# Kernel optimization log

Hardware: AMD Instinct MI355X
Metric: run time of the kernel (lower is better)

The kernel has to match this reference:

```python
import jax, jax.numpy as jnp
import numpy as np

D_MODEL = 768
N_HEADS = 12
D_FF = 3072
EPS = 1e-5


def _layernorm(x, g, b):
    mu = jnp.mean(x, axis=-1, keepdims=True)
    var = jnp.mean(jnp.square(x - mu), axis=-1, keepdims=True)
    return (x - mu) * jax.lax.rsqrt(var + EPS) * g + b


def setup_inputs() -> dict:
    key = jax.random.key(0)
    ks = jax.random.split(key, 16)
    d, f = D_MODEL, D_FF
    s = 1.0 / np.sqrt(d)
    inp = {
        "x": jax.random.normal(ks[0], (1, 4096, d), dtype=jnp.float32),
        "Wq": jax.random.normal(ks[1], (d, d), dtype=jnp.float32) * s,
        "bq": jnp.zeros((d,), jnp.float32),
        "Wk": jax.random.normal(ks[2], (d, d), dtype=jnp.float32) * s,
        "bk": jnp.zeros((d,), jnp.float32),
        "Wv": jax.random.normal(ks[3], (d, d), dtype=jnp.float32) * s,
        "bv": jnp.zeros((d,), jnp.float32),
        "Wo": jax.random.normal(ks[4], (d, d), dtype=jnp.float32) * s,
        "bo": jnp.zeros((d,), jnp.float32),
        "ln1_g": jnp.ones((d,), jnp.float32),
        "ln1_b": jnp.zeros((d,), jnp.float32),
        "ln2_g": jnp.ones((d,), jnp.float32),
        "ln2_b": jnp.zeros((d,), jnp.float32),
        "W1": jax.random.normal(ks[5], (d, f), dtype=jnp.float32) * s,
        "b1": jnp.zeros((f,), jnp.float32),
        "W2": jax.random.normal(ks[6], (f, d), dtype=jnp.float32) * (1.0 / np.sqrt(f)),
        "b2": jnp.zeros((d,), jnp.float32),
    }
    return inp


def reference(x, Wq, bq, Wk, bk, Wv, bv, Wo, bo, ln1_g, ln1_b, ln2_g, ln2_b, W1, b1, W2, b2):
    b, s, d = x.shape
    h = N_HEADS
    dk = d // h

    # --- attention sublayer (pre-norm residual) ---
    xn = _layernorm(x, ln1_g, ln1_b)

    def proj(W, bias):
        y = xn @ W + bias                      # [b, s, d]
        return y.reshape(b, s, h, dk).transpose(0, 2, 1, 3)  # [b, h, s, dk]

    q, k, v = proj(Wq, bq), proj(Wk, bk), proj(Wv, bv)
    scores = jnp.einsum("bhqd,bhkd->bhqk", q, k) / np.sqrt(dk)
    attn = jax.nn.softmax(scores, axis=-1)
    ctx = jnp.einsum("bhqk,bhkd->bhqd", attn, v)
    ctx = ctx.transpose(0, 2, 1, 3).reshape(b, s, d)
    x = x + (ctx @ Wo + bo)

    # --- FFN sublayer (pre-norm residual) ---
    xn2 = _layernorm(x, ln2_g, ln2_b)
    ff = jax.nn.gelu(xn2 @ W1 + b1, approximate=False) @ W2 + b2
    return x + ff
```

## Files before the change

### kernel.cpp

```cpp
#include <hip/hip_runtime.h>
#include <hip/hip_bf16.h>

typedef __attribute__((ext_vector_type(8))) __bf16 bf16x8;
typedef __attribute__((ext_vector_type(4))) __bf16 bf16x4;
typedef __attribute__((ext_vector_type(4))) float f32x4;
typedef __attribute__((ext_vector_type(4))) unsigned short u16x4;
typedef __attribute__((ext_vector_type(8))) unsigned short u16x8;
typedef unsigned short ushort_t;

__device__ __forceinline__ ushort_t f2bf(float f) {
    union { float f; unsigned u; } v; v.f = f;
    unsigned r = v.u + 0x7fffu + ((v.u >> 16) & 1u);
    return (ushort_t)(r >> 16);
}

__device__ __forceinline__ void gload16(const ushort_t* g, ushort_t* l) {
    __builtin_amdgcn_global_load_lds(
        (const __attribute__((address_space(1))) unsigned int*)g,
        (__attribute__((address_space(3))) unsigned int*)l,
        16, 0, 0);
}

__device__ __forceinline__ void ln_row(const float* __restrict__ xr,
                                       const float* __restrict__ g,
                                       const float* __restrict__ b,
                                       ushort_t* __restrict__ orow, int t) {
    float v0 = xr[t], v1 = xr[t + 256], v2 = xr[t + 512];
    float s  = v0 + v1 + v2;
    float s2 = v0 * v0 + v1 * v1 + v2 * v2;
#pragma unroll
    for (int off = 32; off; off >>= 1) {
        s  += __shfl_down(s, off);
        s2 += __shfl_down(s2, off);
    }
    __shared__ float red[8];
    const int wid = t >> 6, lane = t & 63;
    if (lane == 0) { red[wid] = s; red[4 + wid] = s2; }
    __syncthreads();
    __shared__ float stats[2];
    if (t == 0) {
        float S = red[0] + red[1] + red[2] + red[3];
        float S2 = red[4] + red[5] + red[6] + red[7];
        float mu = S * (1.0f / 768.0f);
        float var = S2 * (1.0f / 768.0f) - mu * mu;
        stats[0] = mu;
        stats[1] = rsqrtf(var + 1e-5f);
    }
    __syncthreads();
    const float mu = stats[0], rs = stats[1];
    orow[t]       = f2bf((v0 - mu) * rs * g[t]       + b[t]);
    orow[t + 256] = f2bf((v1 - mu) * rs * g[t + 256] + b[t + 256]);
    orow[t + 512] = f2bf((v2 - mu) * rs * g[t + 512] + b[t + 512]);
}

__global__ __launch_bounds__(256) void ln_kernel(const float* __restrict__ x,
                                                 const float* __restrict__ g,
                                                 const float* __restrict__ b,
                                                 ushort_t* __restrict__ out) {
    const int row = blockIdx.x;
    ln_row(x + (size_t)row * 768, g, b, out + (size_t)row * 768, threadIdx.x);
}

__global__ __launch_bounds__(256) void prep_ln(
    const float* __restrict__ Wq, const float* __restrict__ Wk,
    const float* __restrict__ Wv, const float* __restrict__ Wo,
    const float* __restrict__ W1, const float* __restrict__ W2,
    const float* __restrict__ bq, const float* __restrict__ bk,
    const float* __restrict__ bv,
    const float* __restrict__ x, const float* __restrict__ ln1_g,
    const float* __restrict__ ln1_b,
    ushort_t* __restrict__ WqkvT, ushort_t* __restrict__ WoT,
    ushort_t* __restrict__ W1T, ushort_t* __restrict__ W2T,
    float* __restrict__ bqkv, ushort_t* __restrict__ xn) {
    const int bid = blockIdx.x;
    const int t = threadIdx.x;
    if (bid >= 6915) {
        const int row = bid - 6915;
        ln_row(x + (size_t)row * 768, ln1_g, ln1_b, xn + (size_t)row * 768, t);
        return;
    }
    if (bid >= 6912) {
        const int i = bid - 6912;
        const float* s = (i == 0) ? bq : (i == 1) ? bk : bv;
#pragma unroll
        for (int j = t; j < 768; j += 256) bqkv[i * 768 + j] = s[j];
        return;
    }
    const float* src; ushort_t* dst; int R, C, ti;
    if (bid < 576)       { src = Wq; dst = WqkvT;               R = 768;  C = 768;  ti = bid; }
    else if (bid < 1152) { src = Wk; dst = WqkvT + 768 * 768;   R = 768;  C = 768;  ti = bid - 576; }
    else if (bid < 1728) { src = Wv; dst = WqkvT + 2 * 768 * 768; R = 768; C = 768; ti = bid - 1152; }
    else if (bid < 2304) { src = Wo; dst = WoT;                 R = 768;  C = 768;  ti = bid - 1728; }
    else if (bid < 4608) { src = W1; dst = W1T;                 R = 768;  C = 3072; ti = bid - 2304; }
    else                 { src = W2; dst = W2T;                 R = 3072; C = 768;  ti = bid - 4608; }
    const int tpr = C >> 5;
    const int c0 = (ti % tpr) * 32, r0 = (ti / tpr) * 32;
    __shared__ float tile[32][33];
    {
        const int c = t & 31, r = t >> 5;
#pragma unroll
        for (int i = 0; i < 4; i++)
            tile[r + i * 8][c] = src[(size_t)(r0 + r + i * 8) * C + c0 + c];
    }
    __syncthreads();
    {
        const int oc = t >> 3, q = t & 7;
        u16x4 o;
#pragma unroll
        for (int k = 0; k < 4; k++) o[k] = f2bf(tile[q * 4 + k][oc]);
        *(u16x4*)&dst[(size_t)(c0 + oc) * R + r0 + q * 4] = o;
    }
}

template <int GELU, int RES, int OUTF, int OUTB, int OUTV>
__global__ __launch_bounds__(256, 3)
void gemm64(const ushort_t* __restrict__ A, const ushort_t* __restrict__ Bt,
            const float* __restrict__ bias, const float* __restrict__ res,
            float* __restrict__ outF, ushort_t* __restrict__ outB, int ldo,
            ushort_t* __restrict__ outV,
            int M, int N, int K) {
    constexpr int TR = 192, BK = 64, LL = 6;
    __shared__ __align__(16) ushort_t Ls[2][TR * BK];

    const int nbx = gridDim.x;
    const int nwg = nbx * gridDim.y;
    int fb = blockIdx.y * nbx + blockIdx.x;
    fb = (fb & 7) * (nwg >> 3) + (fb >> 3);
    const int m0 = (fb / nbx) * 128, n0 = (fb % nbx) * 64;

    const int t = threadIdx.x;
    const int wid = t >> 6, lane = t & 63;
    const int wr = wid >> 1, wc = wid & 1;
    const int row16 = lane & 15, kg = lane >> 4;
    const int rsw = row16 & 7;

    const int srow = lane >> 3;
    const int sslot = (lane & 7) ^ srow;
    const ushort_t* gsrc[LL];
    int lofs[LL];
#pragma unroll
    for (int i = 0; i < LL; i++) {
        const int r0 = wid * 48 + 8 * i;
        gsrc[i] = (r0 < 128 ? A + (size_t)(m0 + r0 + srow) * K
                            : Bt + (size_t)(n0 + r0 - 128 + srow) * K) + sslot * 8;
        lofs[i] = r0 * BK;
    }

#define STAGEP(buf, kofs) do {                                       \
        _Pragma("unroll")                                            \
        for (int i = 0; i < LL; i++)                                 \
            gload16(gsrc[i] + (kofs), &Ls[buf][lofs[i]]);            \
    } while (0)

    f32x4 acc[4][2] = {};
    const int NS = K >> 6;
    STAGEP(0, 0);
    STAGEP(1, BK);
    int cur = 0;

    for (int s = 0; s < NS; ++s) {
        if (s + 1 == NS) asm volatile("s_waitcnt vmcnt(0)" ::: "memory");
        else             asm volatile("s_waitcnt vmcnt(%0)" :: "i"(LL) : "memory");
        __builtin_amdgcn_s_barrier();

        bf16x8 a[2][4], b[2][2];
#pragma unroll
        for (int kk = 0; kk < 2; kk++) {
            const int sA = ((kk * 4 + kg) ^ rsw) * 8;
#pragma unroll
            for (int i = 0; i < 4; i++)
                a[kk][i] = *(const bf16x8*)&Ls[cur][(wr * 64 + i * 16 + row16) * BK + sA];
#pragma unroll
            for (int j = 0; j < 2; j++)
                b[kk][j] = *(const bf16x8*)&Ls[cur][(128 + wc * 32 + j * 16 + row16) * BK + sA];
        }
        asm volatile("s_waitcnt lgkmcnt(0)" ::: "memory");
        __builtin_amdgcn_s_barrier();
        if (s + 2 < NS) STAGEP(cur, (s + 2) * BK);

        __builtin_amdgcn_s_setprio(1);
#pragma unroll
        for (int kk = 0; kk < 2; kk++)
#pragma unroll
            for (int i = 0; i < 4; i++)
#pragma unroll
                for (int j = 0; j < 2; j++)
                    acc[i][j] = __builtin_amdgcn_mfma_f32_16x16x32_bf16(a[kk][i], b[kk][j], acc[i][j], 0, 0, 0);
        __builtin_amdgcn_s_setprio(0);
        cur ^= 1;
    }
#undef STAGEP

#pragma unroll
    for (int i = 0; i < 4; i++)
#pragma unroll
        for (int j = 0; j < 2; j++) {
            const int col = n0 + wc * 32 + j * 16 + row16;
            const float bv = bias[col];
            const int rb = m0 + wr * 64 + i * 16 + kg * 4;
            if (OUTV && col >= 1536) {
                bf16x4 pk;
#pragma unroll
                for (int r = 0; r < 4; r++) pk[r] = (__bf16)(acc[i][j][r] + bv);
                *(bf16x4*)&outV[(size_t)(col - 1536) * 4096 + rb] = pk;
            } else {
#pragma unroll
                for (int r = 0; r < 4; r++) {
                    const int row = rb + r;
                    float v = acc[i][j][r] + bv;
                    if (GELU) {
                        float u = v + 0.044715f * v * v * v;
                        float e = __builtin_amdgcn_exp2f(2.30220779f * u);
                        v = v * e * __builtin_amdgcn_rcpf(e + 1.0f);
                    }
                    if (OUTV && col < 768) v *= 0.18033688011112042f;
                    if (RES) v += res[(size_t)row * N + col];
                    if (OUTF) outF[(size_t)row * N + col] = v;
                    if (OUTB) outB[(size_t)row * ldo + col] = f2bf(v);
                }
            }
        }
}

__device__ __forceinline__ int swz(int row, int col) {
    return row * 64 + (col ^ ((row & 7) << 3));
}

__global__ __launch_bounds__(256, 3)
void attn_kernel(const ushort_t* __restrict__ qk,
                 const ushort_t* __restrict__ Vt,
                 ushort_t* __restrict__ num0, ushort_t* __restrict__ num1,
                 float* __restrict__ den) {
    int fb = blockIdx.y * 32 + blockIdx.x;
    fb = (fb & 7) * 96 + (fb >> 3);
    const int q0 = (fb & 31) * 128;
    const int hs = fb >> 5;
    const int h = hs >> 1, sp = hs & 1;
    const int kt0 = sp * 32;

    const int t  = threadIdx.x;
    const int w = t >> 6, lane = t & 63;
    const int row16 = lane & 15, kg = lane >> 4;
    const int kb = kg * 8;

    __shared__ __align__(16) ushort_t Ps[128 * 64];
    __shared__ __align__(16) ushort_t Ks[2][64 * 64];
    __shared__ __align__(16) ushort_t Vs[2][64 * 64];

    {
        const int qr = t >> 1, cb = (t & 1) * 32;
        const size_t qbase = (size_t)(q0 + qr) * 1536 + h * 64 + cb;
#pragma unroll
        for (int j = 0; j < 4; j++)
            *(uint4*)&Ps[swz(qr, cb + j * 8)] = *(const uint4*)&qk[qbase + j * 8];
    }
    {
        const int sr = t >> 2, sc = (t & 3) * 8;
        const size_t kbase = (size_t)(kt0 * 64 + sr) * 1536 + 768 + h * 64 + sc;
        *(uint4*)&Ks[0][swz(sr, sc)]      = *(const uint4*)&qk[kbase];
        *(uint4*)&Ks[0][swz(sr, sc + 32)] = *(const uint4*)&qk[kbase + 32];
        const size_t vbase = (size_t)(h * 64 + sr) * 4096 + kt0 * 64 + sc;
        *(uint4*)&Vs[0][swz(sr, sc)]      = *(const uint4*)&Vt[vbase];
        *(uint4*)&Vs[0][swz(sr, sc + 32)] = *(const uint4*)&Vt[vbase + 32];
    }
    bf16x8 qa0[2], qa1[2];
#pragma unroll
    for (int qb = 0; qb < 2; qb++) {
        qa0[qb] = *(const bf16x8*)&Ps[swz(w * 32 + qb * 16 + row16, kb)];
        qa1[qb] = *(const bf16x8*)&Ps[swz(w * 32 + qb * 16 + row16, 32 + kb)];
    }
    __syncthreads();

    const int rr = lane >> 3;
    const int gcol = ((lane & 7) ^ rr) * 8;
    const ushort_t* gK = qk + 768 + h * 64 + gcol + (size_t)(w * 16 + rr) * 1536;
    const ushort_t* gV = Vt + (size_t)(h * 64 + w * 16 + rr) * 4096 + gcol;

    bf16x8 vones;
#pragma unroll
    for (int i = 0; i < 8; i++) vones[i] = (__bf16)1.0f;

    f32x4 o_acc[2][4] = {};
    f32x4 o_l[2] = {};
    int cur = 0;

    for (int it = 0; it < 32; ++it) {
        if (it != 31) {
            const int kv1 = (kt0 + it + 1) * 64;
            ushort_t* kd = &Ks[cur ^ 1][w * 1024];
            ushort_t* vd = &Vs[cur ^ 1][w * 1024];
            gload16(gK + (size_t)kv1 * 1536,       kd);
            gload16(gK + (size_t)(kv1 + 8) * 1536, kd + 512);
            gload16(gV + kv1,                      vd);
            gload16(gV + kv1 + 8 * 4096,           vd + 512);
        }

        const ushort_t* Kc = Ks[cur];
        const ushort_t* Vc = Vs[cur];

        bf16x8 ka0[4], ka1[4];
#pragma unroll
        for (int f = 0; f < 4; f++) {
            ka0[f] = *(const bf16x8*)&Kc[swz(f * 16 + row16, kb)];
            ka1[f] = *(const bf16x8*)&Kc[swz(f * 16 + row16, 32 + kb)];
        }

        f32x4 s_acc[2][4];
        __builtin_amdgcn_s_setprio(1);
#pragma unroll
        for (int qb = 0; qb < 2; qb++)
#pragma unroll
            for (int f = 0; f < 4; f++) {
                f32x4 z = {};
                z = __builtin_amdgcn_mfma_f32_16x16x32_bf16(ka0[f], qa0[qb], z, 0, 0, 0);
                s_acc[qb][f] = __builtin_amdgcn_mfma_f32_16x16x32_bf16(ka1[f], qa1[qb], z, 0, 0, 0);
            }
        __builtin_amdgcn_s_setprio(0);

#pragma unroll
        for (int qb = 0; qb < 2; qb++)
#pragma unroll
            for (int f = 0; f < 4; f++) {
                bf16x4 pk;
#pragma unroll
                for (int r = 0; r < 4; r++)
                    pk[r] = (__bf16)__builtin_amdgcn_exp2f(fminf(s_acc[qb][f][r], 30.0f));
                *(bf16x4*)&Ps[swz(w * 32 + qb * 16 + row16, f * 16 + kg * 4)] = pk;
            }

        bf16x8 pa0[2], pa1[2];
#pragma unroll
        for (int qb = 0; qb < 2; qb++) {
            pa0[qb] = *(const bf16x8*)&Ps[swz(w * 32 + qb * 16 + row16, kb)];
            pa1[qb] = *(const bf16x8*)&Ps[swz(w * 32 + qb * 16 + row16, 32 + kb)];
        }
        __builtin_amdgcn_s_setprio(1);
#pragma unroll
        for (int f = 0; f < 4; f++) {
            bf16x8 vb0 = *(const bf16x8*)&Vc[swz(f * 16 + row16, kb)];
            bf16x8 vb1 = *(const bf16x8*)&Vc[swz(f * 16 + row16, 32 + kb)];
#pragma unroll
            for (int qb = 0; qb < 2; qb++) {
                o_acc[qb][f] = __builtin_amdgcn_mfma_f32_16x16x32_bf16(pa0[qb], vb0, o_acc[qb][f], 0, 0, 0);
                o_acc[qb][f] = __builtin_amdgcn_mfma_f32_16x16x32_bf16(pa1[qb], vb1, o_acc[qb][f], 0, 0, 0);
            }
        }
#pragma unroll
        for (int qb = 0; qb < 2; qb++) {
            o_l[qb] = __builtin_amdgcn_mfma_f32_16x16x32_bf16(pa0[qb], vones, o_l[qb], 0, 0, 0);
            o_l[qb] = __builtin_amdgcn_mfma_f32_16x16x32_bf16(pa1[qb], vones, o_l[qb], 0, 0, 0);
        }
        __builtin_amdgcn_s_setprio(0);

        __syncthreads();
        cur ^= 1;
    }

    ushort_t* np = sp ? num1 : num0;
#pragma unroll
    for (int qb = 0; qb < 2; qb++)
#pragma unroll
        for (int f = 0; f < 4; f++)
#pragma unroll
            for (int r = 0; r < 4; r++) {
                const int qrow = q0 + w * 32 + qb * 16 + kg * 4 + r;
                np[(size_t)qrow * 768 + h * 64 + f * 16 + row16] = f2bf(o_acc[qb][f][r]);
            }
    if (row16 == 0) {
#pragma unroll
        for (int qb = 0; qb < 2; qb++)
#pragma unroll
            for (int r = 0; r < 4; r++) {
                const int qrow = q0 + w * 32 + qb * 16 + kg * 4 + r;
                den[((size_t)sp * 12 + h) * 4096 + qrow] = o_l[qb][r];
            }
    }
}

__global__ __launch_bounds__(256) void attn_combine(
    const ushort_t* __restrict__ num0, const ushort_t* __restrict__ num1,
    const float* __restrict__ den, ushort_t* __restrict__ ctx) {
    const int idx = blockIdx.x * 256 + threadIdx.x;
    const int q = idx / 96;
    const int g = idx % 96;
    const int h = g >> 3;
    const float rd = __builtin_amdgcn_rcpf(den[(size_t)h * 4096 + q] +
                                           den[((size_t)12 + h) * 4096 + q]);
    const size_t o = (size_t)q * 768 + g * 8;
    u16x8 a = *(const u16x8*)&num0[o];
    u16x8 b = *(const u16x8*)&num1[o];
    u16x8 pk;
#pragma unroll
    for (int i = 0; i < 8; i++) {
        const float av = __uint_as_float((unsigned)a[i] << 16);
        const float bv = __uint_as_float((unsigned)b[i] << 16);
        pk[i] = f2bf((av + bv) * rd);
    }
    *(u16x8*)&ctx[o] = pk;
}

extern "C" void kernel_launch(void* const* d_in, const int* in_sizes, int n_in,
                              void* d_out, int out_size, void* d_ws, size_t ws_size,
                              hipStream_t stream) {
    const float* x     = (const float*)d_in[0];
    const float* Wq    = (const float*)d_in[1];
    const float* bq    = (const float*)d_in[2];
    const float* Wk    = (const float*)d_in[3];
    const float* bk    = (const float*)d_in[4];
    const float* Wv    = (const float*)d_in[5];
    const float* bv    = (const float*)d_in[6];
    const float* Wo    = (const float*)d_in[7];
    const float* bo    = (const float*)d_in[8];
    const float* ln1_g = (const float*)d_in[9];
    const float* ln1_b = (const float*)d_in[10];
    const float* ln2_g = (const float*)d_in[11];
    const float* ln2_b = (const float*)d_in[12];
    const float* W1    = (const float*)d_in[13];
    const float* b1    = (const float*)d_in[14];
    const float* W2    = (const float*)d_in[15];
    const float* b2    = (const float*)d_in[16];

    char* ws = (char*)d_ws;
    ushort_t* WqkvT = (ushort_t*)ws; ws += (size_t)2304 * 768 * 2;
    ushort_t* WoT   = (ushort_t*)ws; ws += (size_t)768 * 768 * 2;
    ushort_t* W1T   = (ushort_t*)ws; ws += (size_t)3072 * 768 * 2;
    ushort_t* W2T   = (ushort_t*)ws; ws += (size_t)768 * 3072 * 2;
    float*    bqkv  = (float*)ws;    ws += (size_t)2304 * 4;
    ushort_t* xn    = (ushort_t*)ws; ws += (size_t)4096 * 768 * 2;
    ushort_t* qk    = (ushort_t*)ws; ws += (size_t)4096 * 1536 * 2;
    ushort_t* Vtb   = (ushort_t*)ws; ws += (size_t)768 * 4096 * 2;
    ushort_t* ctxb  = (ushort_t*)ws; ws += (size_t)4096 * 768 * 2;
    float*    x1    = (float*)ws;    ws += (size_t)4096 * 768 * 4;
    ushort_t* num0b = (ushort_t*)ws; ws += (size_t)4096 * 768 * 2;
    ushort_t* num1b = (ushort_t*)ws; ws += (size_t)4096 * 768 * 2;
    float*    den   = (float*)ws;    ws += (size_t)2 * 12 * 4096 * 4;
    ushort_t* H     = qk;

    prep_ln<<<6915 + 4096, 256, 0, stream>>>(Wq, Wk, Wv, Wo, W1, W2, bq, bk, bv,
                                             x, ln1_g, ln1_b,
                                             WqkvT, WoT, W1T, W2T, bqkv, xn);

    gemm64<0, 0, 0, 1, 1><<<dim3(36, 32), 256, 0, stream>>>(
        xn, WqkvT, bqkv, nullptr, nullptr, qk, 1536, Vtb, 4096, 2304, 768);

    attn_kernel<<<dim3(32, 24), 256, 0, stream>>>(qk, Vtb, num0b, num1b, den);
    attn_combine<<<1536, 256, 0, stream>>>(num0b, num1b, den, ctxb);

    gemm64<0, 1, 1, 0, 0><<<dim3(12, 32), 256, 0, stream>>>(
        ctxb, WoT, bo, x, x1, nullptr, 0, nullptr, 4096, 768, 768);

    ln_kernel<<<4096, 256, 0, stream>>>(x1, ln2_g, ln2_b, xn);
    gemm64<1, 0, 0, 1, 0><<<dim3(48, 32), 256, 0, stream>>>(
        xn, W1T, b1, nullptr, nullptr, H, 3072, nullptr, 4096, 3072, 768);
    gemm64<0, 1, 1, 0, 0><<<dim3(12, 32), 256, 0, stream>>>(
        H, W2T, b2, x1, (float*)d_out, nullptr, 0, nullptr, 4096, 768, 3072);

    (void)in_sizes; (void)n_in; (void)out_size; (void)ws_size;
}
```

Baseline: 190.1 us.

## Split attention KV range four ways and drop double-buffered K/V staging

The attention kernel now splits each head's key range into four chunks instead of two, doubling the grid to 1536 blocks. K/V shared memory drops from double-buffered to single-buffered, with the next tile's async load issued between two barriers after compute, and launch bounds rise to 4 blocks per CU. The combine kernel sums four partial numerators and denominators. This is meant to raise occupancy and parallelism, but it loses the overlap of loads with compute, adds a barrier per iteration, and doubles the partial-result traffic through the combine step.

```diff
diff --git a/kernel.cpp b/kernel.cpp
--- a/kernel.cpp
+++ b/kernel.cpp
@@ -226,17 +226,17 @@
     return row * 64 + (col ^ ((row & 7) << 3));
 }
 
-__global__ __launch_bounds__(256, 3)
+__global__ __launch_bounds__(256, 4)
 void attn_kernel(const ushort_t* __restrict__ qk,
                  const ushort_t* __restrict__ Vt,
-                 ushort_t* __restrict__ num0, ushort_t* __restrict__ num1,
+                 ushort_t* __restrict__ num,
                  float* __restrict__ den) {
     int fb = blockIdx.y * 32 + blockIdx.x;
-    fb = (fb & 7) * 96 + (fb >> 3);
+    fb = (fb & 7) * 192 + (fb >> 3);
     const int q0 = (fb & 31) * 128;
     const int hs = fb >> 5;
-    const int h = hs >> 1, sp = hs & 1;
-    const int kt0 = sp * 32;
+    const int h = hs >> 2, sp = hs & 3;
+    const int kt0 = sp * 16;
 
     const int t  = threadIdx.x;
     const int w = t >> 6, lane = t & 63;
@@ -244,8 +244,8 @@
     const int kb = kg * 8;
 
     __shared__ __align__(16) ushort_t Ps[128 * 64];
-    __shared__ __align__(16) ushort_t Ks[2][64 * 64];
-    __shared__ __align__(16) ushort_t Vs[2][64 * 64];
+    __shared__ __align__(16) ushort_t Ks[64 * 64];
+    __shared__ __align__(16) ushort_t Vs[64 * 64];
 
     {
         const int qr = t >> 1, cb = (t & 1) * 32;
@@ -257,11 +257,11 @@
     {
         const int sr = t >> 2, sc = (t & 3) * 8;
         const size_t kbase = (size_t)(kt0 * 64 + sr) * 1536 + 768 + h * 64 + sc;
-        *(uint4*)&Ks[0][swz(sr, sc)]      = *(const uint4*)&qk[kbase];
-        *(uint4*)&Ks[0][swz(sr, sc + 32)] = *(const uint4*)&qk[kbase + 32];
+        *(uint4*)&Ks[swz(sr, sc)]      = *(const uint4*)&qk[kbase];
+        *(uint4*)&Ks[swz(sr, sc + 32)] = *(const uint4*)&qk[kbase + 32];
         const size_t vbase = (size_t)(h * 64 + sr) * 4096 + kt0 * 64 + sc;
-        *(uint4*)&Vs[0][swz(sr, sc)]      = *(const uint4*)&Vt[vbase];
-        *(uint4*)&Vs[0][swz(sr, sc + 32)] = *(const uint4*)&Vt[vbase + 32];
+        *(uint4*)&Vs[swz(sr, sc)]      = *(const uint4*)&Vt[vbase];
+        *(uint4*)&Vs[swz(sr, sc + 32)] = *(const uint4*)&Vt[vbase + 32];
     }
     bf16x8 qa0[2], qa1[2];
 #pragma unroll
@@ -282,27 +282,13 @@
 
     f32x4 o_acc[2][4] = {};
     f32x4 o_l[2] = {};
-    int cur = 0;
-
-    for (int it = 0; it < 32; ++it) {
-        if (it != 31) {
-            const int kv1 = (kt0 + it + 1) * 64;
-            ushort_t* kd = &Ks[cur ^ 1][w * 1024];
-            ushort_t* vd = &Vs[cur ^ 1][w * 1024];
-            gload16(gK + (size_t)kv1 * 1536,       kd);
-            gload16(gK + (size_t)(kv1 + 8) * 1536, kd + 512);
-            gload16(gV + kv1,                      vd);
-            gload16(gV + kv1 + 8 * 4096,           vd + 512);
-        }
-
-        const ushort_t* Kc = Ks[cur];
-        const ushort_t* Vc = Vs[cur];
-
+
+    for (int it = 0; it < 16; ++it) {
         bf16x8 ka0[4], ka1[4];
 #pragma unroll
         for (int f = 0; f < 4; f++) {
-            ka0[f] = *(const bf16x8*)&Kc[swz(f * 16 + row16, kb)];
-            ka1[f] = *(const bf16x8*)&Kc[swz(f * 16 + row16, 32 + kb)];
+            ka0[f] = *(const bf16x8*)&Ks[swz(f * 16 + row16, kb)];
+            ka1[f] = *(const bf16x8*)&Ks[swz(f * 16 + row16, 32 + kb)];
         }
 
         f32x4 s_acc[2][4];
@@ -337,8 +323,8 @@
         __builtin_amdgcn_s_setprio(1);
 #pragma unroll
         for (int f = 0; f < 4; f++) {
-            bf16x8 vb0 = *(const bf16x8*)&Vc[swz(f * 16 + row16, kb)];
-            bf16x8 vb1 = *(const bf16x8*)&Vc[swz(f * 16 + row16, 32 + kb)];
+            bf16x8 vb0 = *(const bf16x8*)&Vs[swz(f * 16 + row16, kb)];
+            bf16x8 vb1 = *(const bf16x8*)&Vs[swz(f * 16 + row16, 32 + kb)];
 #pragma unroll
             for (int qb = 0; qb < 2; qb++) {
                 o_acc[qb][f] = __builtin_amdgcn_mfma_f32_16x16x32_bf16(pa0[qb], vb0, o_acc[qb][f], 0, 0, 0);
@@ -353,10 +339,17 @@
         __builtin_amdgcn_s_setprio(0);
 
         __syncthreads();
-        cur ^= 1;
-    }
-
-    ushort_t* np = sp ? num1 : num0;
+        if (it != 15) {
+            const int kv1 = (kt0 + it + 1) * 64;
+            gload16(gK + (size_t)kv1 * 1536,       &Ks[w * 1024]);
+            gload16(gK + (size_t)(kv1 + 8) * 1536, &Ks[w * 1024 + 512]);
+            gload16(gV + kv1,                      &Vs[w * 1024]);
+            gload16(gV + kv1 + 8 * 4096,           &Vs[w * 1024 + 512]);
+        }
+        __syncthreads();
+    }
+
+    ushort_t* np = num + (size_t)sp * 4096 * 768;
 #pragma unroll
     for (int qb = 0; qb < 2; qb++)
 #pragma unroll
@@ -378,24 +371,28 @@
 }
 
 __global__ __launch_bounds__(256) void attn_combine(
-    const ushort_t* __restrict__ num0, const ushort_t* __restrict__ num1,
-    const float* __restrict__ den, ushort_t* __restrict__ ctx) {
+    const ushort_t* __restrict__ num, const float* __restrict__ den,
+    ushort_t* __restrict__ ctx) {
     const int idx = blockIdx.x * 256 + threadIdx.x;
     const int q = idx / 96;
     const int g = idx % 96;
     const int h = g >> 3;
-    const float rd = __builtin_amdgcn_rcpf(den[(size_t)h * 4096 + q] +
-                                           den[((size_t)12 + h) * 4096 + q]);
+    float d = 0.0f;
+#pragma unroll
+    for (int sp = 0; sp < 4; sp++) d += den[((size_t)sp * 12 + h) * 4096 + q];
+    const float rd = __builtin_amdgcn_rcpf(d);
     const size_t o = (size_t)q * 768 + g * 8;
-    u16x8 a = *(const u16x8*)&num0[o];
-    u16x8 b = *(const u16x8*)&num1[o];
+    float acc[8] = {};
+#pragma unroll
+    for (int sp = 0; sp < 4; sp++) {
+        u16x8 a = *(const u16x8*)&num[(size_t)sp * 4096 * 768 + o];
+#pragma unroll
+        for (int i = 0; i < 8; i++)
+            acc[i] += __uint_as_float((unsigned)a[i] << 16);
+    }
     u16x8 pk;
 #pragma unroll
-    for (int i = 0; i < 8; i++) {
-        const float av = __uint_as_float((unsigned)a[i] << 16);
-        const float bv = __uint_as_float((unsigned)b[i] << 16);
-        pk[i] = f2bf((av + bv) * rd);
-    }
+    for (int i = 0; i < 8; i++) pk[i] = f2bf(acc[i] * rd);
     *(u16x8*)&ctx[o] = pk;
 }
 
@@ -431,9 +428,8 @@
     ushort_t* Vtb   = (ushort_t*)ws; ws += (size_t)768 * 4096 * 2;
     ushort_t* ctxb  = (ushort_t*)ws; ws += (size_t)4096 * 768 * 2;
     float*    x1    = (float*)ws;    ws += (size_t)4096 * 768 * 4;
-    ushort_t* num0b = (ushort_t*)ws; ws += (size_t)4096 * 768 * 2;
-    ushort_t* num1b = (ushort_t*)ws; ws += (size_t)4096 * 768 * 2;
-    float*    den   = (float*)ws;    ws += (size_t)2 * 12 * 4096 * 4;
+    ushort_t* numb  = (ushort_t*)ws; ws += (size_t)4 * 4096 * 768 * 2;
+    float*    den   = (float*)ws;    ws += (size_t)4 * 12 * 4096 * 4;
     ushort_t* H     = qk;
 
     prep_ln<<<6915 + 4096, 256, 0, stream>>>(Wq, Wk, Wv, Wo, W1, W2, bq, bk, bv,
@@ -443,8 +439,8 @@
     gemm64<0, 0, 0, 1, 1><<<dim3(36, 32), 256, 0, stream>>>(
         xn, WqkvT, bqkv, nullptr, nullptr, qk, 1536, Vtb, 4096, 2304, 768);
 
-    attn_kernel<<<dim3(32, 24), 256, 0, stream>>>(qk, Vtb, num0b, num1b, den);
-    attn_combine<<<1536, 256, 0, stream>>>(num0b, num1b, den, ctxb);
+    attn_kernel<<<dim3(32, 48), 256, 0, stream>>>(qk, Vtb, numb, den);
+    attn_combine<<<1536, 256, 0, stream>>>(numb, den, ctxb);
 
     gemm64<0, 1, 1, 0, 0><<<dim3(12, 32), 256, 0, stream>>>(
         ctxb, WoT, bo, x, x1, nullptr, 0, nullptr, 4096, 768, 768);
```

Measured after the change: 194.4 us. 2.2% more time.
